# Performance work log

Hardware: AMD Instinct MI355X
Metric: run time of the kernel (lower is better)

The kernel has to match this reference:

```python
import jax, jax.numpy as jnp
import numpy as np

V, C, T, H, L, B = 32000, 1024, 1024, 16, 4, 4
HD = C // H
FF = 4 * C
LN_EPS = 1e-5


def _sinusoidal(block_size, n_embd):
    pos = np.arange(block_size, dtype=np.float32)[:, None]
    div = np.exp(np.arange(0, n_embd, 2, dtype=np.float32) * (-np.log(10000.0) / n_embd))
    enc = np.zeros((block_size, n_embd), dtype=np.float32)
    enc[:, 0::2] = np.sin(pos * div)
    enc[:, 1::2] = np.cos(pos * div)
    return jnp.asarray(enc)


def setup_inputs() -> dict:
    key = jax.random.key(0)
    ks = jax.random.split(key, 12)
    std = 0.02
    n = lambda k, s: jax.random.normal(k, s, jnp.float32) * std
    return {
        'idx': jax.random.randint(ks[0], (B, T), 0, V),
        'emb': n(ks[1], (V, C)),
        'pos_enc': _sinusoidal(T, C),
        'Wq': n(ks[2], (L, C, C)),
        'Wk': n(ks[3], (L, C, C)),
        'Wv': n(ks[4], (L, C, C)),
        'Wo': n(ks[5], (L, C, C)),
        'bo': jnp.zeros((L, C), jnp.float32),
        'W1': n(ks[6], (L, C, FF)),
        'b1': jnp.zeros((L, FF), jnp.float32),
        'W2': n(ks[7], (L, FF, C)),
        'b2': jnp.zeros((L, C), jnp.float32),
        'ln1_g': jnp.ones((L, C), jnp.float32),
        'ln1_b': jnp.zeros((L, C), jnp.float32),
        'ln2_g': jnp.ones((L, C), jnp.float32),
        'ln2_b': jnp.zeros((L, C), jnp.float32),
        'lnf_g': jnp.ones((C,), jnp.float32),
        'lnf_b': jnp.zeros((C,), jnp.float32),
        'Wlm': n(ks[8], (C, V)),
        'blm': jnp.zeros((V,), jnp.float32),
    }


def _layer_norm(x, g, b):
    m = jnp.mean(x, -1, keepdims=True)
    v = jnp.var(x, -1, keepdims=True)
    return (x - m) * jax.lax.rsqrt(v + LN_EPS) * g + b


def _forward(idx, emb, pos_enc, Wq, Wk, Wv, Wo, bo, W1, b1, W2, b2,
             ln1_g, ln1_b, ln2_g, ln2_b, lnf_g, lnf_b, Wlm, blm):
    Bv, Tv = idx.shape
    x = emb[idx] + pos_enc[None, :Tv, :]  # [B,T,C]
    mask = jnp.tril(jnp.ones((Tv, Tv), dtype=bool))
    scale = HD ** -0.5

    def block(x, p):
        wq, wk, wv, wo, bov, w1, b1v, w2, b2v, g1, bn1, g2, bn2 = p
        h = _layer_norm(x, g1, bn1)
        q = jnp.einsum('btc,chd->bhtd', h, wq.reshape(C, H, HD))
        k = jnp.einsum('btc,chd->bhtd', h, wk.reshape(C, H, HD))
        v = jnp.einsum('btc,chd->bhtd', h, wv.reshape(C, H, HD))
        wei = jnp.einsum('bhqd,bhkd->bhqk', q, k) * scale
        wei = jnp.where(mask, wei, -jnp.inf)
        wei = jax.nn.softmax(wei, axis=-1)
        o = jnp.einsum('bhqk,bhkd->bhqd', wei, v)
        o = o.transpose(0, 2, 1, 3).reshape(Bv, Tv, C)
        x = x + o @ wo + bov
        h2 = _layer_norm(x, g2, bn2)
        x = x + jax.nn.gelu(h2 @ w1 + b1v, approximate=False) @ w2 + b2v
        return x, None

    x, _ = jax.lax.scan(block, x, (Wq, Wk, Wv, Wo, bo, W1, b1, W2, b2,
                                   ln1_g, ln1_b, ln2_g, ln2_b))
    x = _layer_norm(x, lnf_g, lnf_b)
    return x @ Wlm + blm  # [B,T,V]


def reference(idx, emb, pos_enc, Wq, Wk, Wv, Wo, bo, W1, b1, W2, b2,
              ln1_g, ln1_b, ln2_g, ln2_b, lnf_g, lnf_b, Wlm, blm):
    return _forward(idx, emb, pos_enc, Wq, Wk, Wv, Wo, bo, W1, b1, W2, b2,
                    ln1_g, ln1_b, ln2_g, ln2_b, lnf_g, lnf_b, Wlm, blm)
```

## Files before the change

kernel.cpp:

```cpp
#include <hip/hip_runtime.h>

#define V_  32000
#define C_  1024
#define T_  1024
#define H_  16
#define L_  4
#define B_  4
#define HD_ 64
#define FF_ 4096
#define M_  (B_ * T_)

typedef __attribute__((ext_vector_type(8))) short bf16x8;
typedef __attribute__((ext_vector_type(4))) float f32x4;
typedef unsigned short u16;

#define FENCE() asm volatile("" ::: "memory")
#define BAR()  do { FENCE(); __builtin_amdgcn_s_barrier(); FENCE(); } while (0)
#define VMW(n) asm volatile("s_waitcnt vmcnt(" #n ")" ::: "memory")

__device__ __forceinline__ u16 f2bf(float f) {
  unsigned u = __builtin_bit_cast(unsigned, f);
  u += 0x7fffu + ((u >> 16) & 1u);
  return (u16)(u >> 16);
}

__device__ __forceinline__ void gload16(const u16* g, u16* l) {
  __builtin_amdgcn_global_load_lds(
      (const __attribute__((address_space(1))) void*)g,
      (__attribute__((address_space(3))) void*)l, 16, 0, 0);
}

__global__ __launch_bounds__(256)
void embed_kernel(const int* __restrict__ idx, const float* __restrict__ emb,
                  const float* __restrict__ pos, float* __restrict__ x) {
  int row = blockIdx.x;
  int t = row & (T_ - 1);
  int tok = idx[row];
  float4 e = reinterpret_cast<const float4*>(emb + (size_t)tok * C_)[threadIdx.x];
  float4 p = reinterpret_cast<const float4*>(pos + (size_t)t * C_)[threadIdx.x];
  float4 r;
  r.x = e.x + p.x; r.y = e.y + p.y; r.z = e.z + p.z; r.w = e.w + p.w;
  reinterpret_cast<float4*>(x + (size_t)row * C_)[threadIdx.x] = r;
}

__global__ __launch_bounds__(256)
void ln_kernel(const float* __restrict__ xin, const float* __restrict__ g,
               const float* __restrict__ bta, u16* __restrict__ out) {
  int row = blockIdx.x;
  int tid = threadIdx.x;
  float4 xv = reinterpret_cast<const float4*>(xin + (size_t)row * C_)[tid];
  float s  = xv.x + xv.y + xv.z + xv.w;
  float ss = xv.x * xv.x + xv.y * xv.y + xv.z * xv.z + xv.w * xv.w;
  #pragma unroll
  for (int d = 1; d < 64; d <<= 1) {
    s  += __shfl_xor(s, d, 64);
    ss += __shfl_xor(ss, d, 64);
  }
  __shared__ float rs[4], rss[4];
  int w = tid >> 6, lane = tid & 63;
  if (lane == 0) { rs[w] = s; rss[w] = ss; }
  __syncthreads();
  s  = rs[0] + rs[1] + rs[2] + rs[3];
  ss = rss[0] + rss[1] + rss[2] + rss[3];
  float mean = s * (1.0f / C_);
  float var  = ss * (1.0f / C_) - mean * mean;
  float rstd = rsqrtf(var + 1e-5f);
  float4 gv = reinterpret_cast<const float4*>(g)[tid];
  float4 bv = reinterpret_cast<const float4*>(bta)[tid];
  union { u16 u[4]; uint2 v; } pk;
  pk.u[0] = f2bf((xv.x - mean) * rstd * gv.x + bv.x);
  pk.u[1] = f2bf((xv.y - mean) * rstd * gv.y + bv.y);
  pk.u[2] = f2bf((xv.z - mean) * rstd * gv.z + bv.z);
  pk.u[3] = f2bf((xv.w - mean) * rstd * gv.w + bv.w);
  *reinterpret_cast<uint2*>(&out[(size_t)row * C_ + tid * 4]) = pk.v;
}

__global__ __launch_bounds__(256)
void wtrans_kernel(const float* __restrict__ W, u16* __restrict__ Wt, int K, int N,
                   size_t dstBS) {
  const float* src = W + (size_t)blockIdx.z * K * N;
  u16* dst = Wt + (size_t)blockIdx.z * dstBS;
  __shared__ float tile[32][33];
  int k0 = blockIdx.y * 32, n0 = blockIdx.x * 32;
  int tx = threadIdx.x & 31, ty = threadIdx.x >> 5;
  #pragma unroll
  for (int i = 0; i < 4; ++i)
    tile[ty * 4 + i][tx] = src[(size_t)(k0 + ty * 4 + i) * N + n0 + tx];
  __syncthreads();
  #pragma unroll
  for (int i = 0; i < 4; ++i)
    dst[(size_t)(n0 + ty * 4 + i) * K + k0 + tx] = f2bf(tile[tx][ty * 4 + i]);
}

template <int MODE, int GROUP_M>
__global__ __launch_bounds__(256)
void gemm_bt(const u16* __restrict__ A, const u16* __restrict__ Bt,
             const float* __restrict__ bias, const float* __restrict__ resid,
             void* __restrict__ Cout, u16* __restrict__ vtb,
             int M, int N, int K) {
  __shared__ u16 As[128 * 32];
  __shared__ u16 Bs[128 * 32];
  const int nbm = M >> 7, nbn = N >> 7;
  const int nwg = nbm * nbn;
  const int bid = blockIdx.x;
  const int chunk = nwg >> 3;
  const int swz = (bid & 7) * chunk + (bid >> 3);
  const int gsz = GROUP_M * nbn;
  const int grp = swz / gsz, rem = swz % gsz;
  const int by = grp * GROUP_M + (rem % GROUP_M);
  const int bx = rem / GROUP_M;
  const int m0 = by * 128, n0 = bx * 128;

  const int tid = threadIdx.x, lane = tid & 63, w = tid >> 6;
  const int wr = w >> 1, wc = w & 1;
  const int frow = lane & 15, fk = (lane >> 4) * 8;
  const int srow = lane >> 2, scol = (lane & 3) * 8;

  f32x4 acc[4][4];
  #pragma unroll
  for (int i = 0; i < 4; ++i)
    #pragma unroll
    for (int j = 0; j < 4; ++j) acc[i][j] = (f32x4)0.0f;

  for (int k0 = 0; k0 < K; k0 += 32) {
    gload16(&A [(size_t)(m0 + w * 32 +      srow) * K + k0 + scol], As + w * 1024);
    gload16(&A [(size_t)(m0 + w * 32 + 16 + srow) * K + k0 + scol], As + w * 1024 + 512);
    gload16(&Bt[(size_t)(n0 + w * 32 +      srow) * K + k0 + scol], Bs + w * 1024);
    gload16(&Bt[(size_t)(n0 + w * 32 + 16 + srow) * K + k0 + scol], Bs + w * 1024 + 512);
    __syncthreads();

    bf16x8 af[4], bfr[4];
    #pragma unroll
    for (int mi = 0; mi < 4; ++mi)
      af[mi] = *reinterpret_cast<const bf16x8*>(&As[(wr * 64 + mi * 16 + frow) * 32 + fk]);
    #pragma unroll
    for (int ni = 0; ni < 4; ++ni)
      bfr[ni] = *reinterpret_cast<const bf16x8*>(&Bs[(wc * 64 + ni * 16 + frow) * 32 + fk]);
    #pragma unroll
    for (int mi = 0; mi < 4; ++mi)
      #pragma unroll
      for (int ni = 0; ni < 4; ++ni)
        acc[mi][ni] = __builtin_amdgcn_mfma_f32_16x16x32_bf16(af[mi], bfr[ni], acc[mi][ni], 0, 0, 0);
    __syncthreads();
  }

  u16* outb = (u16*)Cout;
  float* outf = (float*)Cout;
  const bool vblk = (MODE == 4) && (n0 >= 2 * C_);
  #pragma unroll
  for (int mi = 0; mi < 4; ++mi) {
    #pragma unroll
    for (int ni = 0; ni < 4; ++ni) {
      int orow = m0 + wr * 64 + mi * 16 + ((lane >> 4) << 2);
      int ocol = n0 + wc * 64 + ni * 16 + (lane & 15);
      float bv = 0.0f;
      if constexpr (MODE == 1 || MODE == 2 || MODE == 3) bv = bias[ocol];
      if constexpr (MODE == 4) {
        if (vblk) {
          int vcol = ocol - 2 * C_;
          int hh = vcol >> 6, d = vcol & 63;
          int bb = orow >> 10, t0 = orow & (T_ - 1);
          union { u16 u[4]; uint2 v2; } pk;
          #pragma unroll
          for (int r = 0; r < 4; ++r) pk.u[r] = f2bf(acc[mi][ni][r]);
          *reinterpret_cast<uint2*>(
              &vtb[(((size_t)bb * H_ + hh) * HD_ + d) * T_ + t0]) = pk.v2;
        } else {
          #pragma unroll
          for (int r = 0; r < 4; ++r)
            outb[(size_t)(orow + r) * (2 * C_) + ocol] = f2bf(acc[mi][ni][r]);
        }
      } else {
        #pragma unroll
        for (int r = 0; r < 4; ++r) {
          size_t off = (size_t)(orow + r) * N + ocol;
          float val = acc[mi][ni][r] + bv;
          if constexpr (MODE == 0) {
            outb[off] = f2bf(val);
          } else if constexpr (MODE == 1) {
            outf[off] = val + resid[off];
          } else if constexpr (MODE == 2) {
            val = 0.5f * val * (1.0f + erff(val * 0.70710678118654752f));
            outb[off] = f2bf(val);
          } else if constexpr (MODE == 3) {
            outf[off] = val;
          }
        }
      }
    }
  }
}

template <int MODE>
__global__ __launch_bounds__(512, 2)
void gemm8(const u16* __restrict__ A, const u16* __restrict__ Bt,
           const float* __restrict__ bias, const float* __restrict__ resid,
           void* __restrict__ Cout, int M, int N, int K) {
  __shared__ u16 lds8[65536];
  const int nbm = M >> 8, nbn = N >> 8;
  const int nwg = nbm * nbn;
  const int chunk = nwg >> 3;
  const int bid = blockIdx.x;
  const int swz = (bid & 7) * chunk + (bid >> 3);
  const int gsz = 4 * nbn;
  const int grp = swz / gsz, rem = swz % gsz;
  const int by = grp * 4 + (rem & 3);
  const int bx = rem >> 2;
  const int m0 = by << 8, n0 = bx << 8;

  const int tid = threadIdx.x, lane = tid & 63, w = tid >> 6;
  const int wm = w >> 2, wn = w & 3;
  const int fr = lane & 15, kgb = (lane >> 4) * 16;
  const int scolz = 8 * ((lane & 7) ^ (lane >> 3));
  const int NT = K >> 6;
  const int NI = NT >> 1;

  f32x4 acc[8][4];
  #pragma unroll
  for (int i = 0; i < 8; ++i)
    #pragma unroll
    for (int j = 0; j < 4; ++j) acc[i][j] = (f32x4)0.0f;

  auto ldr = [&](int d, int isB, int row, int cb) -> bf16x8 {
    int bo = row * 128 + (cb ^ ((row & 7) << 4));
    const char* base = (const char*)lds8 + d * 65536 + isB * 32768 +
                       (isB ? (wn >> 1) : wm) * 16384;
    return *reinterpret_cast<const bf16x8*>(base + bo);
  };
  auto stage_half = [&](const u16* grow0, u16* ldst) {
    #pragma unroll
    for (int p = 0; p < 2; ++p) {
      int r = (p * 8 + w) * 8 + (lane >> 3);
      gload16(grow0 + (size_t)r * K + scolz, ldst + (p * 8 + w) * 512);
    }
  };
  auto stageA = [&](int d, int h, int t) {
    stage_half(&A[(size_t)(m0 + h * 128) * K + t * 64],
               lds8 + d * 32768 + h * 8192);
  };
  auto stageB = [&](int d, int h, int t) {
    stage_half(&Bt[(size_t)(n0 + h * 128) * K + t * 64],
               lds8 + d * 32768 + 16384 + h * 8192);
  };

  bf16x8 af[2][2], bfr[4][2];

#define LDA_Q(d, q) do {                                   \
    af[0][0] = ldr(d, 0, (q) * 32 + fr,      kgb);         \
    af[0][1] = ldr(d, 0, (q) * 32 + fr,      64 + kgb);    \
    af[1][0] = ldr(d, 0, (q) * 32 + 16 + fr, kgb);         \
    af[1][1] = ldr(d, 0, (q) * 32 + 16 + fr, 64 + kgb);    \
  } while (0)
#define LDB_ALL(d) do {                                    \
    _Pragma("unroll")                                      \
    for (int nj = 0; nj < 4; ++nj) {                       \
      bfr[nj][0] = ldr(d, 1, (wn & 1) * 64 + nj * 16 + fr, kgb);      \
      bfr[nj][1] = ldr(d, 1, (wn & 1) * 64 + nj * 16 + fr, 64 + kgb); \
    }                                                      \
  } while (0)
#define MFMA_Q(q) do {                                     \
    __builtin_amdgcn_s_setprio(1);                         \
    _Pragma("unroll")                                      \
    for (int lmi = 0; lmi < 2; ++lmi)                      \
      _Pragma("unroll")                                    \
      for (int nj = 0; nj < 4; ++nj)                       \
        _Pragma("unroll")                                  \
        for (int ks = 0; ks < 2; ++ks)                     \
          acc[2 * (q) + lmi][nj] = __builtin_amdgcn_mfma_f32_16x16x32_bf16( \
              af[lmi][ks], bfr[nj][ks], acc[2 * (q) + lmi][nj], 0, 0, 0);   \
    __builtin_amdgcn_s_setprio(0);                         \
  } while (0)

  stageB(0, 0, 0); stageB(0, 1, 0);
  stageA(0, 0, 0); stageA(0, 1, 0);
  stageB(1, 0, 1); stageB(1, 1, 1);
  VMW(4);
  BAR();

  for (int i = 0; i < NI; ++i) {
    const int a = 2 * i, b = 2 * i + 1;
    const bool pa = (a + 2 < NT), pb = (b + 2 < NT);
    LDB_ALL(0); LDA_Q(0, 0);
    stageA(1, 0, b);
    BAR(); MFMA_Q(0); BAR();
    LDA_Q(0, 1);
    stageA(1, 1, b);
    if (pa) stageB(0, 0, a + 2);
    BAR(); MFMA_Q(1); BAR();
    LDA_Q(0, 2);
    if (pa) stageB(0, 1, a + 2);
    BAR(); MFMA_Q(2); BAR();
    LDA_Q(0, 3);
    BAR(); MFMA_Q(3);
    if (pa) { VMW(4); } else { VMW(0); }
    BAR();
    LDB_ALL(1); LDA_Q(1, 0);
    if (pa) stageA(0, 0, a + 2);
    BAR(); MFMA_Q(0); BAR();
    LDA_Q(1, 1);
    if (pa) stageA(0, 1, a + 2);
    BAR(); MFMA_Q(1); BAR();
    LDA_Q(1, 2);
    if (pb) stageB(1, 0, b + 2);
    BAR(); MFMA_Q(2); BAR();
    LDA_Q(1, 3);
    if (pb) stageB(1, 1, b + 2);
    BAR(); MFMA_Q(3);
    if (pb) { VMW(4); } else { VMW(0); }
    BAR();
  }
#undef LDA_Q
#undef LDB_ALL
#undef MFMA_Q

  u16* outb = (u16*)Cout;
  float* outf = (float*)Cout;
  #pragma unroll
  for (int mi = 0; mi < 8; ++mi) {
    #pragma unroll
    for (int nj = 0; nj < 4; ++nj) {
      int orow = m0 + wm * 128 + mi * 16 + ((lane >> 4) << 2);
      int ocol = n0 + wn * 64 + nj * 16 + (lane & 15);
      float bv = 0.0f;
      if constexpr (MODE != 0) bv = bias[ocol];
      #pragma unroll
      for (int r = 0; r < 4; ++r) {
        size_t off = (size_t)(orow + r) * N + ocol;
        float val = acc[mi][nj][r] + bv;
        if constexpr (MODE == 0) {
          outb[off] = f2bf(val);
        } else if constexpr (MODE == 1) {
          outf[off] = val + resid[off];
        } else if constexpr (MODE == 2) {
          val = 0.5f * val * (1.0f + erff(val * 0.70710678118654752f));
          outb[off] = f2bf(val);
        } else {
          outf[off] = val;
        }
      }
    }
  }
}

template <int MODE>
__global__ __launch_bounds__(256)
void gemm_legacy(const u16* __restrict__ A, const float* __restrict__ Bw,
                 const float* __restrict__ bias, const float* __restrict__ resid,
                 void* __restrict__ Cout, int M, int N, int K) {
  __shared__ u16 As[128][40];
  __shared__ u16 Bs[128][40];
  const int m0 = blockIdx.y * 128, n0 = blockIdx.x * 128;
  const int tid = threadIdx.x, lane = tid & 63, w = tid >> 6;
  const int wr = w >> 1, wc = w & 1;
  const int row = lane & 15, kk8 = (lane >> 4) * 8;
  f32x4 acc[4][4];
  #pragma unroll
  for (int i = 0; i < 4; ++i)
    #pragma unroll
    for (int j = 0; j < 4; ++j) acc[i][j] = (f32x4)0.0f;
  for (int k0 = 0; k0 < K; k0 += 32) {
    #pragma unroll
    for (int i = 0; i < 2; ++i) {
      int e = (tid + i * 256) * 8;
      int r = e >> 5, c = e & 31;
      *reinterpret_cast<uint4*>(&As[r][c]) =
        *reinterpret_cast<const uint4*>(&A[(size_t)(m0 + r) * K + k0 + c]);
    }
    #pragma unroll
    for (int i = 0; i < 4; ++i) {
      int e = (tid + i * 256) * 4;
      int kr = e >> 7, c = e & 127;
      float4 bv = *reinterpret_cast<const float4*>(&Bw[(size_t)(k0 + kr) * N + n0 + c]);
      Bs[c + 0][kr] = f2bf(bv.x);
      Bs[c + 1][kr] = f2bf(bv.y);
      Bs[c + 2][kr] = f2bf(bv.z);
      Bs[c + 3][kr] = f2bf(bv.w);
    }
    __syncthreads();
    bf16x8 af[4], bfr[4];
    #pragma unroll
    for (int mi = 0; mi < 4; ++mi)
      af[mi] = *reinterpret_cast<const bf16x8*>(&As[wr * 64 + mi * 16 + row][kk8]);
    #pragma unroll
    for (int ni = 0; ni < 4; ++ni)
      bfr[ni] = *reinterpret_cast<const bf16x8*>(&Bs[wc * 64 + ni * 16 + row][kk8]);
    #pragma unroll
    for (int mi = 0; mi < 4; ++mi)
      #pragma unroll
      for (int ni = 0; ni < 4; ++ni)
        acc[mi][ni] = __builtin_amdgcn_mfma_f32_16x16x32_bf16(af[mi], bfr[ni], acc[mi][ni], 0, 0, 0);
    __syncthreads();
  }
  u16* outb = (u16*)Cout;
  float* outf = (float*)Cout;
  #pragma unroll
  for (int mi = 0; mi < 4; ++mi) {
    #pragma unroll
    for (int ni = 0; ni < 4; ++ni) {
      int orow = m0 + wr * 64 + mi * 16 + ((lane >> 4) << 2);
      int ocol = n0 + wc * 64 + ni * 16 + (lane & 15);
      float bv = 0.0f;
      if constexpr (MODE != 0) bv = bias[ocol];
      #pragma unroll
      for (int r = 0; r < 4; ++r) {
        size_t off = (size_t)(orow + r) * N + ocol;
        float val = acc[mi][ni][r] + bv;
        if constexpr (MODE == 0) outb[off] = f2bf(val);
        else if constexpr (MODE == 1) outf[off] = val + resid[off];
        else if constexpr (MODE == 2) {
          val = 0.5f * val * (1.0f + erff(val * 0.70710678118654752f));
          outb[off] = f2bf(val);
        } else outf[off] = val;
      }
    }
  }
}

__global__ __launch_bounds__(256)
void attn_kernel(const u16* __restrict__ qg, const u16* __restrict__ kg,
                 const u16* __restrict__ vt, u16* __restrict__ og) {
  const int bh = blockIdx.y;
  const int q0 = blockIdx.x * 64;
  const int b = bh >> 4;
  const int tid = threadIdx.x, lane = tid & 63, w = tid >> 6;
  const int fr = lane & 15, kk8 = (lane >> 4) * 8;
  __shared__ u16 KS[2][4096];
  __shared__ u16 VS[2][4096];
  __shared__ u16 Ps[4][16][72];

  const int ldq = 2 * C_;
  const size_t baseq = ((size_t)b * T_) * ldq + (bh & 15) * HD_;
  const u16* qbase = qg + baseq;
  const u16* kbase = kg + baseq;
  const u16* vbase = vt + ((size_t)bh * HD_) * T_;
  const size_t baseo = ((size_t)b * T_) * C_ + (bh & 15) * HD_;
  const int qw = q0 + w * 16;

  bf16x8 qf[2];
  #pragma unroll
  for (int s = 0; s < 2; ++s)
    qf[s] = *reinterpret_cast<const bf16x8*>(&qbase[(size_t)(qw + fr) * ldq + s * 32 + kk8]);

  const int srow8 = lane >> 3;
  const int scol = 8 * ((lane & 7) ^ srow8);
  auto stageKV = [&](int d, int kv0) {
    #pragma unroll
    for (int p = 0; p < 2; ++p) {
      int rr = (p * 4 + w) * 8 + srow8;
      gload16(kbase + (size_t)(kv0 + rr) * ldq + scol, &KS[d][(p * 4 + w) * 512]);
      gload16(vbase + (size_t)rr * T_ + kv0 + scol,    &VS[d][(p * 4 + w) * 512]);
    }
  };
  auto ldS = [&](const u16* base, int row, int cu) -> bf16x8 {
    return *reinterpret_cast<const bf16x8*>(&base[row * 64 + (cu ^ ((row & 7) << 3))]);
  };

  f32x4 acc_o[4];
  #pragma unroll
  for (int dt = 0; dt < 4; ++dt) acc_o[dt] = (f32x4)0.0f;
  float m_run[4] = {-1e30f, -1e30f, -1e30f, -1e30f};
  float l_run[4] = {0.f, 0.f, 0.f, 0.f};
  const float scale = 0.125f;

  const int kv_end = q0 + 64;
  stageKV(0, 0);
  VMW(0); BAR();

  int cur = 0;
  for (int kv0 = 0; kv0 < kv_end; kv0 += 64, cur ^= 1) {
    if (kv0 + 64 < kv_end) stageKV(cur ^ 1, kv0 + 64);

    f32x4 sacc[4];
    #pragma unroll
    for (int nt = 0; nt < 4; ++nt) sacc[nt] = (f32x4)0.0f;
    #pragma unroll
    for (int nt = 0; nt < 4; ++nt)
      #pragma unroll
      for (int s = 0; s < 2; ++s) {
        bf16x8 kf = ldS(KS[cur], nt * 16 + fr, s * 32 + kk8);
        sacc[nt] = __builtin_amdgcn_mfma_f32_16x16x32_bf16(qf[s], kf, sacc[nt], 0, 0, 0);
      }

    #pragma unroll
    for (int i = 0; i < 4; ++i) {
      int qrow = qw + ((lane >> 4) << 2) + i;
      float sv[4], pv[4];
      #pragma unroll
      for (int nt = 0; nt < 4; ++nt) {
        sv[nt] = sacc[nt][i] * scale;
        if (kv0 + nt * 16 + (lane & 15) > qrow) sv[nt] = -1e30f;
      }
      float mx = fmaxf(fmaxf(sv[0], sv[1]), fmaxf(sv[2], sv[3]));
      #pragma unroll
      for (int d = 1; d < 16; d <<= 1) mx = fmaxf(mx, __shfl_xor(mx, d, 64));
      float mnew = fmaxf(m_run[i], mx);
      float rsum = 0.0f;
      #pragma unroll
      for (int nt = 0; nt < 4; ++nt) { pv[nt] = __expf(sv[nt] - mnew); rsum += pv[nt]; }
      float alpha = __expf(m_run[i] - mnew);
      #pragma unroll
      for (int d = 1; d < 16; d <<= 1) rsum += __shfl_xor(rsum, d, 64);
      l_run[i] = l_run[i] * alpha + rsum;
      m_run[i] = mnew;
      #pragma unroll
      for (int dt = 0; dt < 4; ++dt) acc_o[dt][i] *= alpha;
      #pragma unroll
      for (int nt = 0; nt < 4; ++nt)
        Ps[w][((lane >> 4) << 2) + i][(lane & 15) + nt * 16] = f2bf(pv[nt]);
    }

    #pragma unroll
    for (int dt = 0; dt < 4; ++dt)
      #pragma unroll
      for (int s = 0; s < 2; ++s) {
        bf16x8 pf = *reinterpret_cast<const bf16x8*>(&Ps[w][fr][s * 32 + kk8]);
        bf16x8 vf = ldS(VS[cur], dt * 16 + fr, s * 32 + kk8);
        acc_o[dt] = __builtin_amdgcn_mfma_f32_16x16x32_bf16(pf, vf, acc_o[dt], 0, 0, 0);
      }
    VMW(0); BAR();
  }

  #pragma unroll
  for (int dt = 0; dt < 4; ++dt)
    #pragma unroll
    for (int i = 0; i < 4; ++i) {
      int r = qw + ((lane >> 4) << 2) + i;
      float val = acc_o[dt][i] / l_run[i];
      og[baseo + (size_t)r * C_ + dt * 16 + (lane & 15)] = f2bf(val);
    }
}

__global__ __launch_bounds__(256)
void attn_legacy(const u16* __restrict__ qg, const u16* __restrict__ kg,
                 const u16* __restrict__ vg, u16* __restrict__ og, int ldq) {
  const int bh = blockIdx.y;
  const int b = bh >> 4, hh = bh & 15;
  const int q0 = blockIdx.x * 64;
  const int tid = threadIdx.x, lane = tid & 63, w = tid >> 6;
  const int row = lane & 15, kk8 = (lane >> 4) * 8;
  __shared__ u16 Ks[64][72];
  __shared__ u16 Vt[64][72];
  __shared__ u16 Ps[4][16][72];

  const size_t basei = ((size_t)b * T_) * ldq + hh * HD_;
  const size_t baseo = ((size_t)b * T_) * C_ + hh * HD_;
  const int qw = q0 + w * 16;

  bf16x8 qf[2];
  #pragma unroll
  for (int s = 0; s < 2; ++s)
    qf[s] = *reinterpret_cast<const bf16x8*>(&qg[basei + (size_t)(qw + row) * ldq + s * 32 + kk8]);

  f32x4 acc_o[4];
  #pragma unroll
  for (int dt = 0; dt < 4; ++dt) acc_o[dt] = (f32x4)0.0f;
  float m_run[4] = {-1e30f, -1e30f, -1e30f, -1e30f};
  float l_run[4] = {0.f, 0.f, 0.f, 0.f};
  const float scale = 0.125f;

  const int sc = (tid & 7) * 8;
  const int kv_end = q0 + 64;
  for (int kv0 = 0; kv0 < kv_end; kv0 += 64) {
    #pragma unroll
    for (int p = 0; p < 2; ++p) {
      int sr = p * 32 + (tid >> 3);
      *reinterpret_cast<uint4*>(&Ks[sr][sc]) =
        *reinterpret_cast<const uint4*>(&kg[basei + (size_t)(kv0 + sr) * ldq + sc]);
      union { uint4 u4; u16 us[8]; } vv;
      vv.u4 = *reinterpret_cast<const uint4*>(&vg[basei + (size_t)(kv0 + sr) * ldq + sc]);
      #pragma unroll
      for (int j = 0; j < 8; ++j) Vt[sc + j][sr] = vv.us[j];
    }
    __syncthreads();

    f32x4 sacc[4];
    #pragma unroll
    for (int nt = 0; nt < 4; ++nt) sacc[nt] = (f32x4)0.0f;
    #pragma unroll
    for (int nt = 0; nt < 4; ++nt)
      #pragma unroll
      for (int s = 0; s < 2; ++s) {
        bf16x8 kf = *reinterpret_cast<const bf16x8*>(&Ks[nt * 16 + row][s * 32 + kk8]);
        sacc[nt] = __builtin_amdgcn_mfma_f32_16x16x32_bf16(qf[s], kf, sacc[nt], 0, 0, 0);
      }

    #pragma unroll
    for (int i = 0; i < 4; ++i) {
      int qrow = qw + ((lane >> 4) << 2) + i;
      float sv[4], pv[4];
      #pragma unroll
      for (int nt = 0; nt < 4; ++nt) {
        sv[nt] = sacc[nt][i] * scale;
        if (kv0 + nt * 16 + (lane & 15) > qrow) sv[nt] = -1e30f;
      }
      float mx = fmaxf(fmaxf(sv[0], sv[1]), fmaxf(sv[2], sv[3]));
      #pragma unroll
      for (int d = 1; d < 16; d <<= 1) mx = fmaxf(mx, __shfl_xor(mx, d, 64));
      float mnew = fmaxf(m_run[i], mx);
      float rsum = 0.0f;
      #pragma unroll
      for (int nt = 0; nt < 4; ++nt) { pv[nt] = __expf(sv[nt] - mnew); rsum += pv[nt]; }
      float alpha = __expf(m_run[i] - mnew);
      #pragma unroll
      for (int d = 1; d < 16; d <<= 1) rsum += __shfl_xor(rsum, d, 64);
      l_run[i] = l_run[i] * alpha + rsum;
      m_run[i] = mnew;
      #pragma unroll
      for (int dt = 0; dt < 4; ++dt) acc_o[dt][i] *= alpha;
      #pragma unroll
      for (int nt = 0; nt < 4; ++nt)
        Ps[w][((lane >> 4) << 2) + i][(lane & 15) + nt * 16] = f2bf(pv[nt]);
    }

    #pragma unroll
    for (int dt = 0; dt < 4; ++dt)
      #pragma unroll
      for (int s = 0; s < 2; ++s) {
        bf16x8 pf = *reinterpret_cast<const bf16x8*>(&Ps[w][row][s * 32 + kk8]);
        bf16x8 vf = *reinterpret_cast<const bf16x8*>(&Vt[dt * 16 + row][s * 32 + kk8]);
        acc_o[dt] = __builtin_amdgcn_mfma_f32_16x16x32_bf16(pf, vf, acc_o[dt], 0, 0, 0);
      }
    __syncthreads();
  }

  #pragma unroll
  for (int dt = 0; dt < 4; ++dt)
    #pragma unroll
    for (int i = 0; i < 4; ++i) {
      int r = qw + ((lane >> 4) << 2) + i;
      float val = acc_o[dt][i] / l_run[i];
      og[baseo + (size_t)r * C_ + dt * 16 + (lane & 15)] = f2bf(val);
    }
}

extern "C" void kernel_launch(void* const* d_in, const int* in_sizes, int n_in,
                              void* d_out, int out_size, void* d_ws, size_t ws_size,
                              hipStream_t stream) {
  const int*   idx  = (const int*)d_in[0];
  const float* emb  = (const float*)d_in[1];
  const float* pos  = (const float*)d_in[2];
  const float* Wq   = (const float*)d_in[3];
  const float* Wk   = (const float*)d_in[4];
  const float* Wv   = (const float*)d_in[5];
  const float* Wo   = (const float*)d_in[6];
  const float* bo   = (const float*)d_in[7];
  const float* W1   = (const float*)d_in[8];
  const float* b1   = (const float*)d_in[9];
  const float* W2   = (const float*)d_in[10];
  const float* b2   = (const float*)d_in[11];
  const float* ln1g = (const float*)d_in[12];
  const float* ln1b = (const float*)d_in[13];
  const float* ln2g = (const float*)d_in[14];
  const float* ln2b = (const float*)d_in[15];
  const float* lnfg = (const float*)d_in[16];
  const float* lnfb = (const float*)d_in[17];
  const float* Wlm  = (const float*)d_in[18];
  const float* blm  = (const float*)d_in[19];

  char* ws = (char*)d_ws;
  float* x    = (float*)ws;
  u16*   h    = (u16*)(ws + (16u << 20));
  u16*   qkv  = (u16*)(ws + (24u << 20));
  u16*   vtb  = (u16*)(ws + (40u << 20));
  u16*   ob   = (u16*)(ws + (48u << 20));
  u16*   ffb  = (u16*)(ws + (24u << 20));

  u16* WqkvT = (u16*)(ws + (56u  << 20));
  u16* WoT   = (u16*)(ws + (80u  << 20));
  u16* W1T   = (u16*)(ws + (88u  << 20));
  u16* W2T   = (u16*)(ws + (120u << 20));
  u16* WlmT  = (u16*)(ws + (152u << 20));
  const size_t WS_NEED = (152ull << 20) + 2ull * C_ * V_;

  dim3 blk(256), blk8(512);
  const int nQKV = (M_ / 128) * (3 * C_ / 128);
  const int nCC  = (M_ / 128) * (C_ / 128);
  const int nF1_8 = (M_ / 256) * (FF_ / 256);
  const int nLM_8 = (M_ / 256) * (V_ / 256);
  dim3 gA(T_ / 64, B_ * H_);

  embed_kernel<<<M_, blk, 0, stream>>>(idx, emb, pos, x);

  if (ws_size >= WS_NEED) {
    const size_t s3 = (size_t)3 * C_ * C_;
    wtrans_kernel<<<dim3(C_ / 32,  C_ / 32, L_), blk, 0, stream>>>(Wq, WqkvT,              C_, C_, s3);
    wtrans_kernel<<<dim3(C_ / 32,  C_ / 32, L_), blk, 0, stream>>>(Wk, WqkvT + (size_t)C_ * C_,     C_, C_, s3);
    wtrans_kernel<<<dim3(C_ / 32,  C_ / 32, L_), blk, 0, stream>>>(Wv, WqkvT + (size_t)2 * C_ * C_, C_, C_, s3);
    wtrans_kernel<<<dim3(C_ / 32,  C_ / 32, L_), blk, 0, stream>>>(Wo, WoT, C_, C_, (size_t)C_ * C_);
    wtrans_kernel<<<dim3(FF_ / 32, C_ / 32, L_), blk, 0, stream>>>(W1, W1T, C_, FF_, (size_t)C_ * FF_);
    wtrans_kernel<<<dim3(C_ / 32, FF_ / 32, L_), blk, 0, stream>>>(W2, W2T, FF_, C_, (size_t)C_ * FF_);
    wtrans_kernel<<<dim3(V_ / 32,  C_ / 32, 1),  blk, 0, stream>>>(Wlm, WlmT, C_, V_, (size_t)C_ * V_);

    for (int l = 0; l < L_; ++l) {
      ln_kernel<<<M_, blk, 0, stream>>>(x, ln1g + l * C_, ln1b + l * C_, h);
      gemm_bt<4, 8><<<nQKV, blk, 0, stream>>>(h, WqkvT + (size_t)l * s3, nullptr, nullptr, qkv, vtb, M_, 3 * C_, C_);
      attn_kernel<<<gA, blk, 0, stream>>>(qkv, qkv + C_, vtb, ob);
      gemm_bt<1, 8><<<nCC, blk, 0, stream>>>(ob, WoT + (size_t)l * C_ * C_, bo + l * C_, x, x, nullptr, M_, C_, C_);
      ln_kernel<<<M_, blk, 0, stream>>>(x, ln2g + l * C_, ln2b + l * C_, h);
      gemm8<2><<<nF1_8, blk8, 0, stream>>>(h, W1T + (size_t)l * C_ * FF_, b1 + l * FF_, nullptr, ffb, M_, FF_, C_);
      gemm_bt<1, 8><<<nCC, blk, 0, stream>>>(ffb, W2T + (size_t)l * C_ * FF_, b2 + l * C_, x, x, nullptr, M_, C_, FF_);
    }
    ln_kernel<<<M_, blk, 0, stream>>>(x, lnfg, lnfb, h);
    gemm8<3><<<nLM_8, blk8, 0, stream>>>(h, WlmT, blm, nullptr, (float*)d_out, M_, V_, C_);
  } else {
    float* xr = x;
    u16* qb = qkv;
    u16* kb = qkv + (size_t)M_ * C_;
    u16* vb = (u16*)(ws + (40u << 20));
    dim3 gC(C_ / 128, M_ / 128);
    dim3 gF(FF_ / 128, M_ / 128);
    dim3 gV(V_ / 128, M_ / 128);
    for (int l = 0; l < L_; ++l) {
      ln_kernel<<<M_, blk, 0, stream>>>(xr, ln1g + l * C_, ln1b + l * C_, h);
      gemm_legacy<0><<<gC, blk, 0, stream>>>(h, Wq + (size_t)l * C_ * C_, nullptr, nullptr, qb, M_, C_, C_);
      gemm_legacy<0><<<gC, blk, 0, stream>>>(h, Wk + (size_t)l * C_ * C_, nullptr, nullptr, kb, M_, C_, C_);
      gemm_legacy<0><<<gC, blk, 0, stream>>>(h, Wv + (size_t)l * C_ * C_, nullptr, nullptr, vb, M_, C_, C_);
      attn_legacy<<<gA, blk, 0, stream>>>(qb, kb, vb, ob, C_);
      gemm_legacy<1><<<gC, blk, 0, stream>>>(ob, Wo + (size_t)l * C_ * C_, bo + l * C_, xr, xr, M_, C_, C_);
      ln_kernel<<<M_, blk, 0, stream>>>(xr, ln2g + l * C_, ln2b + l * C_, h);
      gemm_legacy<2><<<gF, blk, 0, stream>>>(h, W1 + (size_t)l * C_ * FF_, b1 + l * FF_, nullptr, ffb, M_, FF_, C_);
      gemm_legacy<1><<<gC, blk, 0, stream>>>(ffb, W2 + (size_t)l * FF_ * C_, b2 + l * C_, xr, xr, M_, C_, FF_);
    }
    ln_kernel<<<M_, blk, 0, stream>>>(xr, lnfg, lnfb, h);
    gemm_legacy<3><<<gV, blk, 0, stream>>>(h, Wlm, blm, nullptr, (float*)d_out, M_, V_, C_);
  }
}
```

Before: 1.675 ms.

## Widen attention blocks to 128 queries, wave-per-row layernorm, vectorized transpose stores

Attention now uses 512-thread blocks covering 128 queries, so each staged K/V tile is shared by 8 waves instead of 4. This halves the global K/V reloads per head, at the cost of extra masked work on the diagonal and fewer blocks in flight. LayerNorm assigns one wave per row and drops the shared-memory reduction and block barrier. The weight transpose writes 4 packed bf16 values per store instead of scalar stores.

```diff
diff --git a/kernel.cpp b/kernel.cpp
--- a/kernel.cpp
+++ b/kernel.cpp
@@ -46,33 +46,36 @@
 __global__ __launch_bounds__(256)
 void ln_kernel(const float* __restrict__ xin, const float* __restrict__ g,
                const float* __restrict__ bta, u16* __restrict__ out) {
-  int row = blockIdx.x;
-  int tid = threadIdx.x;
-  float4 xv = reinterpret_cast<const float4*>(xin + (size_t)row * C_)[tid];
-  float s  = xv.x + xv.y + xv.z + xv.w;
-  float ss = xv.x * xv.x + xv.y * xv.y + xv.z * xv.z + xv.w * xv.w;
+  const int w = threadIdx.x >> 6, lane = threadIdx.x & 63;
+  const int row = blockIdx.x * 4 + w;
+  const float4* xr = reinterpret_cast<const float4*>(xin + (size_t)row * C_);
+  float4 xv[4];
+  float s = 0.f, ss = 0.f;
+  #pragma unroll
+  for (int j = 0; j < 4; ++j) {
+    xv[j] = xr[lane + 64 * j];
+    s  += xv[j].x + xv[j].y + xv[j].z + xv[j].w;
+    ss += xv[j].x * xv[j].x + xv[j].y * xv[j].y + xv[j].z * xv[j].z + xv[j].w * xv[j].w;
+  }
   #pragma unroll
   for (int d = 1; d < 64; d <<= 1) {
     s  += __shfl_xor(s, d, 64);
     ss += __shfl_xor(ss, d, 64);
   }
-  __shared__ float rs[4], rss[4];
-  int w = tid >> 6, lane = tid & 63;
-  if (lane == 0) { rs[w] = s; rss[w] = ss; }
-  __syncthreads();
-  s  = rs[0] + rs[1] + rs[2] + rs[3];
-  ss = rss[0] + rss[1] + rss[2] + rss[3];
   float mean = s * (1.0f / C_);
   float var  = ss * (1.0f / C_) - mean * mean;
   float rstd = rsqrtf(var + 1e-5f);
-  float4 gv = reinterpret_cast<const float4*>(g)[tid];
-  float4 bv = reinterpret_cast<const float4*>(bta)[tid];
-  union { u16 u[4]; uint2 v; } pk;
-  pk.u[0] = f2bf((xv.x - mean) * rstd * gv.x + bv.x);
-  pk.u[1] = f2bf((xv.y - mean) * rstd * gv.y + bv.y);
-  pk.u[2] = f2bf((xv.z - mean) * rstd * gv.z + bv.z);
-  pk.u[3] = f2bf((xv.w - mean) * rstd * gv.w + bv.w);
-  *reinterpret_cast<uint2*>(&out[(size_t)row * C_ + tid * 4]) = pk.v;
+  #pragma unroll
+  for (int j = 0; j < 4; ++j) {
+    float4 gv = reinterpret_cast<const float4*>(g)[lane + 64 * j];
+    float4 bv = reinterpret_cast<const float4*>(bta)[lane + 64 * j];
+    union { u16 u[4]; uint2 v; } pk;
+    pk.u[0] = f2bf((xv[j].x - mean) * rstd * gv.x + bv.x);
+    pk.u[1] = f2bf((xv[j].y - mean) * rstd * gv.y + bv.y);
+    pk.u[2] = f2bf((xv[j].z - mean) * rstd * gv.z + bv.z);
+    pk.u[3] = f2bf((xv[j].w - mean) * rstd * gv.w + bv.w);
+    *reinterpret_cast<uint2*>(&out[(size_t)row * C_ + (lane + 64 * j) * 4]) = pk.v;
+  }
 }
 
 __global__ __launch_bounds__(256)
@@ -87,9 +90,11 @@
   for (int i = 0; i < 4; ++i)
     tile[ty * 4 + i][tx] = src[(size_t)(k0 + ty * 4 + i) * N + n0 + tx];
   __syncthreads();
-  #pragma unroll
-  for (int i = 0; i < 4; ++i)
-    dst[(size_t)(n0 + ty * 4 + i) * K + k0 + tx] = f2bf(tile[tx][ty * 4 + i]);
+  int n = threadIdx.x >> 3, q = threadIdx.x & 7;
+  union { u16 u[4]; uint2 v; } pk;
+  #pragma unroll
+  for (int j = 0; j < 4; ++j) pk.u[j] = f2bf(tile[4 * q + j][n]);
+  *reinterpret_cast<uint2*>(&dst[(size_t)(n0 + n) * K + k0 + 4 * q]) = pk.v;
 }
 
 template <int MODE, int GROUP_M>
@@ -416,17 +421,17 @@
   }
 }
 
-__global__ __launch_bounds__(256)
+__global__ __launch_bounds__(512)
 void attn_kernel(const u16* __restrict__ qg, const u16* __restrict__ kg,
                  const u16* __restrict__ vt, u16* __restrict__ og) {
   const int bh = blockIdx.y;
-  const int q0 = blockIdx.x * 64;
+  const int q0 = blockIdx.x * 128;
   const int b = bh >> 4;
   const int tid = threadIdx.x, lane = tid & 63, w = tid >> 6;
   const int fr = lane & 15, kk8 = (lane >> 4) * 8;
   __shared__ u16 KS[2][4096];
   __shared__ u16 VS[2][4096];
-  __shared__ u16 Ps[4][16][72];
+  __shared__ u16 Ps[8][16][72];
 
   const int ldq = 2 * C_;
   const size_t baseq = ((size_t)b * T_) * ldq + (bh & 15) * HD_;
@@ -444,12 +449,9 @@
   const int srow8 = lane >> 3;
   const int scol = 8 * ((lane & 7) ^ srow8);
   auto stageKV = [&](int d, int kv0) {
-    #pragma unroll
-    for (int p = 0; p < 2; ++p) {
-      int rr = (p * 4 + w) * 8 + srow8;
-      gload16(kbase + (size_t)(kv0 + rr) * ldq + scol, &KS[d][(p * 4 + w) * 512]);
-      gload16(vbase + (size_t)rr * T_ + kv0 + scol,    &VS[d][(p * 4 + w) * 512]);
-    }
+    int rr = w * 8 + srow8;
+    gload16(kbase + (size_t)(kv0 + rr) * ldq + scol, &KS[d][w * 512]);
+    gload16(vbase + (size_t)rr * T_ + kv0 + scol,    &VS[d][w * 512]);
   };
   auto ldS = [&](const u16* base, int row, int cu) -> bf16x8 {
     return *reinterpret_cast<const bf16x8*>(&base[row * 64 + (cu ^ ((row & 7) << 3))]);
@@ -462,7 +464,7 @@
   float l_run[4] = {0.f, 0.f, 0.f, 0.f};
   const float scale = 0.125f;
 
-  const int kv_end = q0 + 64;
+  const int kv_end = q0 + 128;
   stageKV(0, 0);
   VMW(0); BAR();
 
@@ -672,12 +674,12 @@
   u16* WlmT  = (u16*)(ws + (152u << 20));
   const size_t WS_NEED = (152ull << 20) + 2ull * C_ * V_;
 
-  dim3 blk(256), blk8(512);
+  dim3 blk(256), blk8(512), blkA(512);
   const int nQKV = (M_ / 128) * (3 * C_ / 128);
   const int nCC  = (M_ / 128) * (C_ / 128);
   const int nF1_8 = (M_ / 256) * (FF_ / 256);
   const int nLM_8 = (M_ / 256) * (V_ / 256);
-  dim3 gA(T_ / 64, B_ * H_);
+  dim3 gA(T_ / 128, B_ * H_);
 
   embed_kernel<<<M_, blk, 0, stream>>>(idx, emb, pos, x);
 
@@ -692,15 +694,15 @@
     wtrans_kernel<<<dim3(V_ / 32,  C_ / 32, 1),  blk, 0, stream>>>(Wlm, WlmT, C_, V_, (size_t)C_ * V_);
 
     for (int l = 0; l < L_; ++l) {
-      ln_kernel<<<M_, blk, 0, stream>>>(x, ln1g + l * C_, ln1b + l * C_, h);
+      ln_kernel<<<M_ / 4, blk, 0, stream>>>(x, ln1g + l * C_, ln1b + l * C_, h);
       gemm_bt<4, 8><<<nQKV, blk, 0, stream>>>(h, WqkvT + (size_t)l * s3, nullptr, nullptr, qkv, vtb, M_, 3 * C_, C_);
-      attn_kernel<<<gA, blk, 0, stream>>>(qkv, qkv + C_, vtb, ob);
+      attn_kernel<<<gA, blkA, 0, stream>>>(qkv, qkv + C_, vtb, ob);
       gemm_bt<1, 8><<<nCC, blk, 0, stream>>>(ob, WoT + (size_t)l * C_ * C_, bo + l * C_, x, x, nullptr, M_, C_, C_);
-      ln_kernel<<<M_, blk, 0, stream>>>(x, ln2g + l * C_, ln2b + l * C_, h);
+      ln_kernel<<<M_ / 4, blk, 0, stream>>>(x, ln2g + l * C_, ln2b + l * C_, h);
       gemm8<2><<<nF1_8, blk8, 0, stream>>>(h, W1T + (size_t)l * C_ * FF_, b1 + l * FF_, nullptr, ffb, M_, FF_, C_);
       gemm_bt<1, 8><<<nCC, blk, 0, stream>>>(ffb, W2T + (size_t)l * C_ * FF_, b2 + l * C_, x, x, nullptr, M_, C_, FF_);
     }
-    ln_kernel<<<M_, blk, 0, stream>>>(x, lnfg, lnfb, h);
+    ln_kernel<<<M_ / 4, blk, 0, stream>>>(x, lnfg, lnfb, h);
     gemm8<3><<<nLM_8, blk8, 0, stream>>>(h, WlmT, blm, nullptr, (float*)d_out, M_, V_, C_);
   } else {
     float* xr = x;
@@ -710,18 +712,19 @@
     dim3 gC(C_ / 128, M_ / 128);
     dim3 gF(FF_ / 128, M_ / 128);
     dim3 gV(V_ / 128, M_ / 128);
+    dim3 gAl(T_ / 64, B_ * H_);
     for (int l = 0; l < L_; ++l) {
-      ln_kernel<<<M_, blk, 0, stream>>>(xr, ln1g + l * C_, ln1b + l * C_, h);
+      ln_kernel<<<M_ / 4, blk, 0, stream>>>(xr, ln1g + l * C_, ln1b + l * C_, h);
       gemm_legacy<0><<<gC, blk, 0, stream>>>(h, Wq + (size_t)l * C_ * C_, nullptr, nullptr, qb, M_, C_, C_);
       gemm_legacy<0><<<gC, blk, 0, stream>>>(h, Wk + (size_t)l * C_ * C_, nullptr, nullptr, kb, M_, C_, C_);
       gemm_legacy<0><<<gC, blk, 0, stream>>>(h, Wv + (size_t)l * C_ * C_, nullptr, nullptr, vb, M_, C_, C_);
-      attn_legacy<<<gA, blk, 0, stream>>>(qb, kb, vb, ob, C_);
+      attn_legacy<<<gAl, blk, 0, stream>>>(qb, kb, vb, ob, C_);
       gemm_legacy<1><<<gC, blk, 0, stream>>>(ob, Wo + (size_t)l * C_ * C_, bo + l * C_, xr, xr, M_, C_, C_);
-      ln_kernel<<<M_, blk, 0, stream>>>(xr, ln2g + l * C_, ln2b + l * C_, h);
+      ln_kernel<<<M_ / 4, blk, 0, stream>>>(xr, ln2g + l * C_, ln2b + l * C_, h);
       gemm_legacy<2><<<gF, blk, 0, stream>>>(h, W1 + (size_t)l * C_ * FF_, b1 + l * FF_, nullptr, ffb, M_, FF_, C_);
       gemm_legacy<1><<<gC, blk, 0, stream>>>(ffb, W2 + (size_t)l * FF_ * C_, b2 + l * C_, xr, xr, M_, C_, FF_);
     }
-    ln_kernel<<<M_, blk, 0, stream>>>(xr, lnfg, lnfb, h);
+    ln_kernel<<<M_ / 4, blk, 0, stream>>>(xr, lnfg, lnfb, h);
     gemm_legacy<3><<<gV, blk, 0, stream>>>(h, Wlm, blm, nullptr, (float*)d_out, M_, V_, C_);
   }
 }
```

New measurement: 1.609 ms. -3.9%, faster.
